# Kernel tuning notes

Hardware: AMD Instinct MI355X
Metric: run time of the kernel (lower is better)

## Reference

```python
import jax, jax.numpy as jnp
import numpy as np

B, CIN, COUT, H, W = 8, 8, 16, 256, 256

def setup_inputs() -> dict:
    key = jax.random.key(0)
    k1, k2, k3 = jax.random.split(key, 3)
    x = jax.random.normal(k1, (B, CIN, H, W), dtype=jnp.float32)
    bin_centers = jax.random.normal(k2, (COUT, CIN), dtype=jnp.float32)
    bin_widths = jax.random.normal(k3, (COUT, CIN), dtype=jnp.float32)
    return {"x": x, "bin_centers": bin_centers, "bin_widths": bin_widths}

def reference(x, bin_centers, bin_widths):
    # Gaussian RBF soft-histogram: hist[b,o,h,w] = sum_j exp(-(x[b,j,h,w]-c[o,j])^2 / (2*w[o,j]^2))
    # Original torch code builds hist but (buggily) returns x; we return hist,
    # the actual computation of interest (the nested-loop accumulation).
    diff = x[:, None, :, :, :] - bin_centers[None, :, :, None, None]      # [B,Cout,Cin,H,W]
    inv_two_var = 1.0 / (2.0 * bin_widths[None, :, :, None, None] ** 2)
    hist = jnp.sum(jnp.exp(-(diff ** 2) * inv_two_var), axis=2)           # [B,Cout,H,W]
    return hist
```

## Files before the change

kernel.cpp:

```cpp
#include <hip/hip_runtime.h>


constexpr int CIN   = 8;
constexpr int COUT  = 16;
constexpr int HW    = 256 * 256;
constexpr int BATCH = 8;

__global__ __launch_bounds__(256, 8) void rbf_hist_kernel(
    const float* __restrict__ x,
    const float* __restrict__ centers,
    const float* __restrict__ widths,
    float* __restrict__ out)
{
    __shared__ float2 s_cn[COUT * CIN];

    const int tid = threadIdx.x;
    if (tid < COUT * CIN) {
        float w = widths[tid];
        float negk = -1.4426950408889634f / (2.0f * w * w);
        s_cn[tid] = make_float2(centers[tid], negk);
    }
    __syncthreads();

    const int t = blockIdx.x * 256 + tid;
    const int b = t >> 16;
    const int p = t & (HW - 1);

    const float* __restrict__ xb = x + (b * CIN) * HW + p;
    float xr[CIN];
#pragma unroll
    for (int j = 0; j < CIN; ++j) {
        xr[j] = xb[j * HW];
    }

    float* __restrict__ ob = out + (b * COUT) * HW + p;

#pragma unroll 2
    for (int o = 0; o < COUT; ++o) {
        float acc = 0.f;
#pragma unroll
        for (int j = 0; j < CIN; ++j) {
            const float2 cn = s_cn[o * CIN + j];
            const float d = xr[j] - cn.x;
            acc += __builtin_amdgcn_exp2f((cn.y * d) * d);
        }
        ob[o * HW] = acc;
    }
}

extern "C" void kernel_launch(void* const* d_in, const int* in_sizes, int n_in,
                              void* d_out, int out_size, void* d_ws, size_t ws_size,
                              hipStream_t stream) {
    const float* x       = (const float*)d_in[0];
    const float* centers = (const float*)d_in[1];
    const float* widths  = (const float*)d_in[2];
    float* out           = (float*)d_out;

    const int total_threads = BATCH * HW;
    const int block = 256;
    const int grid  = total_threads / block;

    rbf_hist_kernel<<<grid, block, 0, stream>>>(x, centers, widths, out);
}
```

Baseline: 82.30 us.

## Precompute RBF coefficients in separate kernel and process two pixels per thread

Moves the center and inverse-variance preparation into a tiny precompute kernel that writes float2 pairs to workspace, so the main kernel drops its shared-memory staging and __syncthreads. Each thread now loads and stores float2 (two pixels), halving the thread count and widening memory accesses. Coefficients are read from global memory through uniform loads and cache instead of LDS. The extra launch adds a small fixed overhead and the kernel now depends on the workspace buffer.

```diff
diff --git a/kernel.cpp b/kernel.cpp
--- a/kernel.cpp
+++ b/kernel.cpp
@@ -4,47 +4,50 @@
 constexpr int CIN   = 8;
 constexpr int COUT  = 16;
 constexpr int HW    = 256 * 256;
+constexpr int HW2   = HW / 2;
 constexpr int BATCH = 8;
+
+__global__ __launch_bounds__(128) void rbf_precompute_kernel(
+    const float* __restrict__ centers,
+    const float* __restrict__ widths,
+    float2* __restrict__ cw)
+{
+    const int i = threadIdx.x;
+    const float w = widths[i];
+    const float negk = -1.4426950408889634f / (2.0f * w * w);
+    cw[i] = make_float2(-centers[i], negk);
+}
 
 __global__ __launch_bounds__(256, 8) void rbf_hist_kernel(
     const float* __restrict__ x,
-    const float* __restrict__ centers,
-    const float* __restrict__ widths,
+    const float2* __restrict__ cw,
     float* __restrict__ out)
 {
-    __shared__ float2 s_cn[COUT * CIN];
+    const int t  = blockIdx.x * 256 + threadIdx.x;
+    const int b  = t >> 15;
+    const int p2 = t & (HW2 - 1);
 
-    const int tid = threadIdx.x;
-    if (tid < COUT * CIN) {
-        float w = widths[tid];
-        float negk = -1.4426950408889634f / (2.0f * w * w);
-        s_cn[tid] = make_float2(centers[tid], negk);
-    }
-    __syncthreads();
+    const float2* __restrict__ xv = (const float2*)x;
+    float2* __restrict__ ov = (float2*)out;
 
-    const int t = blockIdx.x * 256 + tid;
-    const int b = t >> 16;
-    const int p = t & (HW - 1);
-
-    const float* __restrict__ xb = x + (b * CIN) * HW + p;
-    float xr[CIN];
+    float2 xr[CIN];
 #pragma unroll
     for (int j = 0; j < CIN; ++j) {
-        xr[j] = xb[j * HW];
+        xr[j] = xv[(b * CIN + j) * HW2 + p2];
     }
-
-    float* __restrict__ ob = out + (b * COUT) * HW + p;
 
 #pragma unroll 2
     for (int o = 0; o < COUT; ++o) {
-        float acc = 0.f;
+        float2 acc = make_float2(0.f, 0.f);
 #pragma unroll
         for (int j = 0; j < CIN; ++j) {
-            const float2 cn = s_cn[o * CIN + j];
-            const float d = xr[j] - cn.x;
-            acc += __builtin_amdgcn_exp2f((cn.y * d) * d);
+            const float2 k = cw[o * CIN + j];
+            const float d0 = xr[j].x + k.x;
+            const float d1 = xr[j].y + k.x;
+            acc.x += __builtin_amdgcn_exp2f((k.y * d0) * d0);
+            acc.y += __builtin_amdgcn_exp2f((k.y * d1) * d1);
         }
-        ob[o * HW] = acc;
+        ov[(b * COUT + o) * HW2 + p2] = acc;
     }
 }
 
@@ -55,10 +58,13 @@
     const float* centers = (const float*)d_in[1];
     const float* widths  = (const float*)d_in[2];
     float* out           = (float*)d_out;
+    float2* cw           = (float2*)d_ws;
 
-    const int total_threads = BATCH * HW;
+    rbf_precompute_kernel<<<1, 128, 0, stream>>>(centers, widths, cw);
+
+    const int total_threads = BATCH * HW2;
     const int block = 256;
     const int grid  = total_threads / block;
 
-    rbf_hist_kernel<<<grid, block, 0, stream>>>(x, centers, widths, out);
+    rbf_hist_kernel<<<grid, block, 0, stream>>>(x, cw, out);
 }
```

New measurement: 105.3 us. +28.0%, slower.
